# Performance work log

Measured on AMD Instinct MI355X. Metric: run time of the kernel, lower is better.

Reference implementation:

```python
import jax, jax.numpy as jnp
import numpy as np

GROUP = 128          # GPTQ quantization group size
H = 2048             # hidden_size
I = 1408             # moe_intermediate_size
T = 16384            # routed tokens


def _pack_rows(v):
    # v: [in, out] int4 values -> [in//8, out] int32 (8 nibbles per int32 along input dim)
    v = v.reshape(v.shape[0] // 8, 8, v.shape[1]).astype(jnp.int32)
    sh = (4 * jnp.arange(8, dtype=jnp.int32))[None, :, None]
    return (v << sh).sum(axis=1).astype(jnp.int32)


def _pack_cols(v):
    # v: [groups, out] int4 values -> [groups, out//8] int32
    v = v.reshape(v.shape[0], v.shape[1] // 8, 8).astype(jnp.int32)
    sh = (4 * jnp.arange(8, dtype=jnp.int32))[None, None, :]
    return (v << sh).sum(axis=-1).astype(jnp.int32)


def _unpack_rows(qw):
    # [in//8, out] int32 -> [in, out] int4 values
    sh = 4 * jnp.arange(8, dtype=jnp.int32)
    v = (qw[:, None, :] >> sh[None, :, None]) & 0xF
    return v.reshape(qw.shape[0] * 8, qw.shape[1])


def _unpack_cols(qz):
    # [groups, out//8] int32 -> [groups, out] int4 values
    sh = 4 * jnp.arange(8, dtype=jnp.int32)
    v = (qz[:, :, None] >> sh[None, None, :]) & 0xF
    return v.reshape(qz.shape[0], qz.shape[1] * 8)


def _dequant(qw, qz, sc):
    # GPTQ dequant: W[k, n] = (q[k, n] - (zero[g(k), n] + 1)) * scale[g(k), n]
    w = _unpack_rows(qw).astype(sc.dtype)                      # [in, out]
    z = (_unpack_cols(qz) + 1).astype(sc.dtype)                # [groups, out]
    scale = jnp.repeat(sc, GROUP, axis=0)                      # [in, out]
    zero = jnp.repeat(z, GROUP, axis=0)                        # [in, out]
    return (w - zero) * scale


def setup_inputs() -> dict:
    key = jax.random.key(0)
    ks = jax.random.split(key, 10)
    x = jax.random.normal(ks[0], (T, H), dtype=jnp.float32)

    def make_quant(kq, kz, ksc, n_in, n_out):
        q = jax.random.randint(kq, (n_in, n_out), 0, 16, dtype=jnp.int32)
        z = jax.random.randint(kz, (n_in // GROUP, n_out), 0, 15, dtype=jnp.int32)
        sc = jax.random.uniform(ksc, (n_in // GROUP, n_out), dtype=jnp.float32,
                                minval=1e-3, maxval=2e-2)
        return _pack_rows(q), _pack_cols(z), sc

    qw_g, qz_g, sc_g = make_quant(ks[1], ks[2], ks[3], H, I)
    qw_u, qz_u, sc_u = make_quant(ks[4], ks[5], ks[6], H, I)
    qw_d, qz_d, sc_d = make_quant(ks[7], ks[8], ks[9], I, H)
    return {"x": x,
            "qw_gate": qw_g, "qz_gate": qz_g, "sc_gate": sc_g,
            "qw_up": qw_u, "qz_up": qz_u, "sc_up": sc_u,
            "qw_down": qw_d, "qz_down": qz_d, "sc_down": sc_d}


def reference(x, qw_gate, qz_gate, sc_gate, qw_up, qz_up, sc_up,
              qw_down, qz_down, sc_down):
    Wg = _dequant(qw_gate, qz_gate, sc_gate)   # [H, I]
    Wu = _dequant(qw_up, qz_up, sc_up)         # [H, I]
    Wd = _dequant(qw_down, qz_down, sc_down)   # [I, H]
    # fused_gate_up: silu(x @ Wg) * (x @ Wu)
    h = jax.nn.silu(x @ Wg) * (x @ Wu)         # [T, I]
    return h @ Wd                              # [T, H]
```

## Files before the change

### kernel.cpp

```cpp
#include <hip/hip_runtime.h>

#define T_DIM 16384
#define H_DIM 2048
#define I_DIM 1408
#define NB_DIM (2 * I_DIM)

typedef _Float16 half8 __attribute__((ext_vector_type(8)));
typedef float floatx4 __attribute__((ext_vector_type(4)));

__device__ __forceinline__ void async_cp16(const _Float16* gp, _Float16* lp) {
    __builtin_amdgcn_global_load_lds(
        (const __attribute__((address_space(1))) unsigned int*)gp,
        (__attribute__((address_space(3))) unsigned int*)lp,
        16, 0, 0);
}

__global__ void cvt_fp16_kernel(const float* __restrict__ x, _Float16* __restrict__ xh) {
    int i = (blockIdx.x * 256 + threadIdx.x) * 8;
    const float4* p = (const float4*)(x + i);
    float4 a = p[0];
    float4 b = p[1];
    half8 o = { (_Float16)a.x, (_Float16)a.y, (_Float16)a.z, (_Float16)a.w,
                (_Float16)b.x, (_Float16)b.y, (_Float16)b.z, (_Float16)b.w };
    *(half8*)(xh + i) = o;
}

__global__ void dequant_kernel(const int* __restrict__ qw, const int* __restrict__ qz,
                               const float* __restrict__ sc, _Float16* __restrict__ Wt,
                               int K, int N, int interleave, int off) {
    __shared__ half8 tile[256];
    int t = threadIdx.x;
    int nl = t & 63, kl = t >> 6;
    int n  = blockIdx.x * 64 + nl;
    int kp = blockIdx.y * 4 + kl;
    int q = qw[kp * N + n];
    int g = kp >> 4;
    float scale = sc[g * N + n];
    int zq = (qz[g * (N >> 3) + (n >> 3)] >> (4 * (n & 7))) & 0xF;
    float zf = (float)(zq + 1);
    half8 o;
#pragma unroll
    for (int j = 0; j < 8; ++j)
        o[j] = (_Float16)(((float)((q >> (4 * j)) & 0xF) - zf) * scale);
    tile[nl * 4 + kl] = o;
    __syncthreads();
    int nl2 = t >> 2, kl2 = t & 3;
    int n2 = blockIdx.x * 64 + nl2;
    int np = interleave ? (((n2 >> 5) << 6) + (n2 & 31) + off) : n2;
    *(half8*)(Wt + (size_t)np * K + (size_t)(blockIdx.y * 4 + kl2) * 8) = tile[nl2 * 4 + kl2];
}


#define STAGE_A(p, h, kt) do {                                                        \
    async_cp16(ag + (size_t)((h) * 128) * KDIM + (size_t)(kt) * 64,                   \
               &As[p][(h) * 8192 + ldst]);                                            \
    async_cp16(ag + (size_t)((h) * 128 + 64) * KDIM + (size_t)(kt) * 64,              \
               &As[p][(h) * 8192 + 4096 + ldst]);                                     \
} while (0)

#define STAGE_B(p, h, kt) do {                                                        \
    async_cp16(bg + (size_t)((h) * 128) * KDIM + (size_t)(kt) * 64,                   \
               &Bs[p][(h) * 8192 + ldst]);                                            \
    async_cp16(bg + (size_t)((h) * 128 + 64) * KDIM + (size_t)(kt) * 64,              \
               &Bs[p][(h) * 8192 + 4096 + ldst]);                                     \
} while (0)

#define PHASE(p, mh, nh, RA, RB, STAGE_STMT, WAIT_STMT) do {                          \
    if (RA) {                                                                         \
        _Pragma("unroll") for (int i_ = 0; i_ < 4; ++i_)                              \
        _Pragma("unroll") for (int kk_ = 0; kk_ < 2; ++kk_)                           \
            af[i_][kk_] = *(const half8*)&As[p][(mh) * 4096 + (aoff[i_] ^ (kk_ * 32))]; \
    }                                                                                 \
    if (RB) {                                                                         \
        _Pragma("unroll") for (int j_ = 0; j_ < 2; ++j_)                              \
        _Pragma("unroll") for (int kk_ = 0; kk_ < 2; ++kk_)                           \
            bf[nh][j_][kk_] = *(const half8*)&Bs[p][(nh) * 2048 + (boff[j_] ^ (kk_ * 32))]; \
    }                                                                                 \
    STAGE_STMT;                                                                       \
    __builtin_amdgcn_s_barrier();                                                     \
    asm volatile("s_waitcnt lgkmcnt(0)" ::: "memory");                                \
    __builtin_amdgcn_s_setprio(1);                                                    \
    _Pragma("unroll") for (int kk_ = 0; kk_ < 2; ++kk_)                               \
    _Pragma("unroll") for (int i_ = 0; i_ < 4; ++i_)                                  \
    _Pragma("unroll") for (int j_ = 0; j_ < 2; ++j_)                                  \
        acc[(mh) * 4 + i_][(nh) * 2 + j_] = __builtin_amdgcn_mfma_f32_16x16x32_f16(   \
            af[i_][kk_], bf[nh][j_][kk_], acc[(mh) * 4 + i_][(nh) * 2 + j_], 0, 0, 0);\
    __builtin_amdgcn_s_setprio(0);                                                    \
    WAIT_STMT;                                                                        \
    __builtin_amdgcn_s_barrier();                                                     \
} while (0)

#define VM(n) asm volatile("s_waitcnt vmcnt(" #n ")" ::: "memory")

#define TILE_FULL(p, kt) do {                                                         \
    PHASE(p, 0, 0, 1, 1, STAGE_A(p ^ 1, 1, (kt) + 1), VM(6));                         \
    PHASE(p, 0, 1, 0, 1, STAGE_B(p ^ 1, 1, (kt) + 1), );                              \
    PHASE(p, 1, 0, 1, 0, STAGE_B(p, 0, (kt) + 2), );                                  \
    PHASE(p, 1, 1, 0, 0, STAGE_A(p, 0, (kt) + 2), VM(8));                             \
} while (0)

#define TILE_PEN(kt) do {                                                             \
    PHASE(0, 0, 0, 1, 1, STAGE_A(1, 1, (kt) + 1), VM(6));                             \
    PHASE(0, 0, 1, 0, 1, STAGE_B(1, 1, (kt) + 1), );                                  \
    PHASE(0, 1, 0, 1, 0, , );                                                         \
    PHASE(0, 1, 1, 0, 0, , VM(4));                                                    \
} while (0)

#define TILE_LAST() do {                                                              \
    PHASE(1, 0, 0, 1, 1, , VM(0));                                                    \
    PHASE(1, 0, 1, 0, 1, , );                                                         \
    PHASE(1, 1, 0, 1, 0, , );                                                         \
    PHASE(1, 1, 1, 0, 0, , );                                                         \
} while (0)

template<int KDIM, int EPI>
__launch_bounds__(512, 2)
__global__ void gemm256(const _Float16* __restrict__ A,
                        const _Float16* __restrict__ B,
                        void* __restrict__ Cout) {
    constexpr int NT = KDIM / 64;
    __shared__ __align__(16) _Float16 As[2][16384];
    __shared__ __align__(16) _Float16 Bs[2][16384];

    const int t = threadIdx.x;
    const int wave = t >> 6, lane = t & 63;
    const int id = blockIdx.x;
    const int m0 = (id & 63) * 256;
    const int n_p = id >> 6;
    const int n0 = n_p * 256;
    const int wm = wave >> 2, wn = wave & 3;
    const int q4 = lane >> 4, l15 = lane & 15;

    const int srow = wave * 8 + (lane >> 3);
    const int schunk = (lane & 7) ^ (lane >> 3);
    const _Float16* ag = A + (size_t)(m0 + srow) * KDIM + schunk * 8;
    const _Float16* bg = B + (size_t)(n0 + srow) * KDIM + schunk * 8;
    const int ldst = wave * 512;

    int aoff[4], boff[2];
#pragma unroll
    for (int i = 0; i < 4; ++i) {
        int rA = wm * 128 + i * 16 + l15;
        aoff[i] = rA * 64 + ((q4 ^ (rA & 7)) * 8);
    }
#pragma unroll
    for (int j = 0; j < 2; ++j) {
        int rB = wn * 64 + j * 16 + l15;
        boff[j] = rB * 64 + ((q4 ^ (rB & 7)) * 8);
    }

    floatx4 zero = {0.f, 0.f, 0.f, 0.f};
    floatx4 acc[8][4];
#pragma unroll
    for (int mi = 0; mi < 8; ++mi)
#pragma unroll
        for (int ni = 0; ni < 4; ++ni) acc[mi][ni] = zero;

    half8 af[4][2];
    half8 bf[2][2][2];

    STAGE_B(0, 0, 0);
    STAGE_A(0, 0, 0);
    STAGE_A(0, 1, 0);
    STAGE_B(0, 1, 0);
    STAGE_B(1, 0, 1);
    STAGE_A(1, 0, 1);
    VM(8);
    __builtin_amdgcn_s_barrier();

    for (int tt = 0; tt < NT - 2; tt += 2) {
        TILE_FULL(0, tt);
        TILE_FULL(1, tt + 1);
    }
    TILE_PEN(NT - 2);
    TILE_LAST();

    if constexpr (EPI == 1) {
        _Float16* hout = (_Float16*)Cout;
        const int rbase = m0 + wm * 128 + q4 * 4;
        const int colbase = (n_p * 4 + wn) * 32 + l15;
#pragma unroll
        for (int mi = 0; mi < 8; ++mi)
#pragma unroll
            for (int nc = 0; nc < 2; ++nc)
#pragma unroll
                for (int r = 0; r < 4; ++r) {
                    int row = rbase + mi * 16 + r;
                    int col = colbase + nc * 16;
                    float g = acc[mi][nc][r];
                    float u = acc[mi][nc + 2][r];
                    float s = (g / (1.0f + __expf(-g))) * u;
                    hout[(size_t)row * I_DIM + col] = (_Float16)s;
                }
    } else {
        float* outp = (float*)Cout;
        const int rbase = m0 + wm * 128 + q4 * 4;
#pragma unroll
        for (int mi = 0; mi < 8; ++mi)
#pragma unroll
            for (int ni = 0; ni < 4; ++ni)
#pragma unroll
                for (int r = 0; r < 4; ++r) {
                    int row = rbase + mi * 16 + r;
                    int col = n0 + wn * 64 + ni * 16 + l15;
                    outp[(size_t)row * H_DIM + col] = acc[mi][ni][r];
                }
    }
}

extern "C" void kernel_launch(void* const* d_in, const int* in_sizes, int n_in,
                              void* d_out, int out_size, void* d_ws, size_t ws_size,
                              hipStream_t stream) {
    const float* x    = (const float*)d_in[0];
    const int* qw_g   = (const int*)d_in[1];
    const int* qz_g   = (const int*)d_in[2];
    const float* sc_g = (const float*)d_in[3];
    const int* qw_u   = (const int*)d_in[4];
    const int* qz_u   = (const int*)d_in[5];
    const float* sc_u = (const float*)d_in[6];
    const int* qw_d   = (const int*)d_in[7];
    const int* qz_d   = (const int*)d_in[8];
    const float* sc_d = (const float*)d_in[9];
    float* out = (float*)d_out;

    char* ws = (char*)d_ws;
    _Float16* xh  = (_Float16*)ws;  ws += (size_t)T_DIM * H_DIM * sizeof(_Float16);
    _Float16* hh  = (_Float16*)ws;  ws += (size_t)T_DIM * I_DIM * sizeof(_Float16);
    _Float16* Bgu = (_Float16*)ws;  ws += (size_t)NB_DIM * H_DIM * sizeof(_Float16);
    _Float16* Wd  = (_Float16*)ws;  ws += (size_t)I_DIM * H_DIM * sizeof(_Float16);

    cvt_fp16_kernel<<<(T_DIM * H_DIM) / 2048, 256, 0, stream>>>(x, xh);
    dequant_kernel<<<dim3(I_DIM / 64, H_DIM / 32), 256, 0, stream>>>(qw_g, qz_g, sc_g, Bgu, H_DIM, I_DIM, 1, 0);
    dequant_kernel<<<dim3(I_DIM / 64, H_DIM / 32), 256, 0, stream>>>(qw_u, qz_u, sc_u, Bgu, H_DIM, I_DIM, 1, 32);
    dequant_kernel<<<dim3(H_DIM / 64, I_DIM / 32), 256, 0, stream>>>(qw_d, qz_d, sc_d, Wd, I_DIM, H_DIM, 0, 0);
    gemm256<H_DIM, 1><<<(T_DIM / 256) * (NB_DIM / 256), 512, 0, stream>>>(xh, Bgu, hh);
    gemm256<I_DIM, 0><<<(T_DIM / 256) * (H_DIM / 256), 512, 0, stream>>>(hh, Wd, out);
}
```

Measured before the change: 497.8 us.

## Restructure GEMM main loop with inline-asm LDS reads and reordered prefetch schedule

```diff
diff --git a/kernel.cpp b/kernel.cpp
--- a/kernel.cpp
+++ b/kernel.cpp
@@ -51,66 +51,69 @@
 }
 
 
-#define STAGE_A(p, h, kt) do {                                                        \
-    async_cp16(ag + (size_t)((h) * 128) * KDIM + (size_t)(kt) * 64,                   \
-               &As[p][(h) * 8192 + ldst]);                                            \
-    async_cp16(ag + (size_t)((h) * 128 + 64) * KDIM + (size_t)(kt) * 64,              \
-               &As[p][(h) * 8192 + 4096 + ldst]);                                     \
-} while (0)
-
-#define STAGE_B(p, h, kt) do {                                                        \
+#define STAGE_A2(pp, sub, kt) do {                                                    \
+    async_cp16(ag + (size_t)((sub) * 64) * KDIM + (size_t)(kt) * 64,                  \
+               &As[pp][(sub) * 4096 + ldst]);                                         \
+    async_cp16(ag + (size_t)(128 + (sub) * 64) * KDIM + (size_t)(kt) * 64,            \
+               &As[pp][8192 + (sub) * 4096 + ldst]);                                  \
+} while (0)
+
+#define STAGE_B(pp, h, kt) do {                                                       \
     async_cp16(bg + (size_t)((h) * 128) * KDIM + (size_t)(kt) * 64,                   \
-               &Bs[p][(h) * 8192 + ldst]);                                            \
+               &Bs[pp][(h) * 8192 + ldst]);                                           \
     async_cp16(bg + (size_t)((h) * 128 + 64) * KDIM + (size_t)(kt) * 64,              \
-               &Bs[p][(h) * 8192 + 4096 + ldst]);                                     \
-} while (0)
-
-#define PHASE(p, mh, nh, RA, RB, STAGE_STMT, WAIT_STMT) do {                          \
-    if (RA) {                                                                         \
-        _Pragma("unroll") for (int i_ = 0; i_ < 4; ++i_)                              \
-        _Pragma("unroll") for (int kk_ = 0; kk_ < 2; ++kk_)                           \
-            af[i_][kk_] = *(const half8*)&As[p][(mh) * 4096 + (aoff[i_] ^ (kk_ * 32))]; \
+               &Bs[pp][(h) * 8192 + 4096 + ldst]);                                    \
+} while (0)
+
+#define DSR(dst, a, OFF) \
+    asm volatile("ds_read_b128 %0, %1 offset:%2" : "=v"(dst) : "v"(a), "n"(OFF) : "memory")
+
+#define READ_A(pp, mh) do {                                                           \
+    _Pragma("unroll") for (int i_ = 0; i_ < 4; ++i_) {                                \
+        DSR(af[i_][0], aw[i_][0], (pp) * 32768 + (mh) * 8192);                        \
+        DSR(af[i_][1], aw[i_][1], (pp) * 32768 + (mh) * 8192);                        \
     }                                                                                 \
-    if (RB) {                                                                         \
-        _Pragma("unroll") for (int j_ = 0; j_ < 2; ++j_)                              \
-        _Pragma("unroll") for (int kk_ = 0; kk_ < 2; ++kk_)                           \
-            bf[nh][j_][kk_] = *(const half8*)&Bs[p][(nh) * 2048 + (boff[j_] ^ (kk_ * 32))]; \
+} while (0)
+
+#define READ_B(pp, nh) do {                                                           \
+    _Pragma("unroll") for (int j_ = 0; j_ < 2; ++j_) {                                \
+        DSR(bf[nh][j_][0], bw[j_][0], (pp) * 32768 + (nh) * 4096);                    \
+        DSR(bf[nh][j_][1], bw[j_][1], (pp) * 32768 + (nh) * 4096);                    \
     }                                                                                 \
-    STAGE_STMT;                                                                       \
-    __builtin_amdgcn_s_barrier();                                                     \
-    asm volatile("s_waitcnt lgkmcnt(0)" ::: "memory");                                \
-    __builtin_amdgcn_s_setprio(1);                                                    \
+} while (0)
+
+#define MFMA16(mh, nh)                                                                \
     _Pragma("unroll") for (int kk_ = 0; kk_ < 2; ++kk_)                               \
     _Pragma("unroll") for (int i_ = 0; i_ < 4; ++i_)                                  \
     _Pragma("unroll") for (int j_ = 0; j_ < 2; ++j_)                                  \
         acc[(mh) * 4 + i_][(nh) * 2 + j_] = __builtin_amdgcn_mfma_f32_16x16x32_f16(   \
-            af[i_][kk_], bf[nh][j_][kk_], acc[(mh) * 4 + i_][(nh) * 2 + j_], 0, 0, 0);\
-    __builtin_amdgcn_s_setprio(0);                                                    \
-    WAIT_STMT;                                                                        \
-    __builtin_amdgcn_s_barrier();                                                     \
-} while (0)
-
+            af[i_][kk_], bf[nh][j_][kk_], acc[(mh) * 4 + i_][(nh) * 2 + j_], 0, 0, 0)
+
+#define LG(n) asm volatile("s_waitcnt lgkmcnt(" #n ")" ::: "memory")
 #define VM(n) asm volatile("s_waitcnt vmcnt(" #n ")" ::: "memory")
+#define BAR __builtin_amdgcn_s_barrier()
+#define SB0 __builtin_amdgcn_sched_barrier(0)
+#define PRIO1 __builtin_amdgcn_s_setprio(1)
+#define PRIO0 __builtin_amdgcn_s_setprio(0)
 
 #define TILE_FULL(p, kt) do {                                                         \
-    PHASE(p, 0, 0, 1, 1, STAGE_A(p ^ 1, 1, (kt) + 1), VM(6));                         \
-    PHASE(p, 0, 1, 0, 1, STAGE_B(p ^ 1, 1, (kt) + 1), );                              \
-    PHASE(p, 1, 0, 1, 0, STAGE_B(p, 0, (kt) + 2), );                                  \
-    PHASE(p, 1, 1, 0, 0, STAGE_A(p, 0, (kt) + 2), VM(8));                             \
-} while (0)
-
-#define TILE_PEN(kt) do {                                                             \
-    PHASE(0, 0, 0, 1, 1, STAGE_A(1, 1, (kt) + 1), VM(6));                             \
-    PHASE(0, 0, 1, 0, 1, STAGE_B(1, 1, (kt) + 1), );                                  \
-    PHASE(0, 1, 0, 1, 0, , );                                                         \
-    PHASE(0, 1, 1, 0, 0, , VM(4));                                                    \
+     STAGE_A2(p ^ 1, 0, (kt) + 1);                                           \
+    BAR; LG(4); SB0; PRIO1; MFMA16(0, 0); PRIO0; SB0;                                 \
+     STAGE_B(p ^ 1, 0, (kt) + 1); STAGE_B(p ^ 1, 1, (kt) + 1);               \
+    VM(6); BAR; LG(0); SB0; PRIO1; MFMA16(0, 1); PRIO0; SB0;                          \
+    READ_A(p, 1);                                                                     \
+     STAGE_A2(p ^ 1, 1, (kt) + 1);                                           \
+    BAR; LG(0); SB0; PRIO1; MFMA16(1, 0); PRIO0; SB0;                                 \
+     VM(2); BAR; LG(0); SB0; PRIO1; MFMA16(1, 1); PRIO0; SB0;                \
+    READ_A(p ^ 1, 0); READ_B(p ^ 1, 0); READ_B(p ^ 1, 1);                             \
 } while (0)
 
 #define TILE_LAST() do {                                                              \
-    PHASE(1, 0, 0, 1, 1, , VM(0));                                                    \
-    PHASE(1, 0, 1, 0, 1, , );                                                         \
-    PHASE(1, 1, 0, 1, 0, , );                                                         \
-    PHASE(1, 1, 1, 0, 0, , );                                                         \
+    BAR; LG(4); SB0; PRIO1; MFMA16(0, 0); PRIO0; SB0;                                 \
+    VM(0); BAR; LG(0); SB0; PRIO1; MFMA16(0, 1); PRIO0; SB0;                          \
+    READ_A(1, 1);                                                                     \
+    BAR; LG(0); SB0; PRIO1; MFMA16(1, 0); PRIO0; SB0;                                 \
+    BAR; LG(0); SB0; PRIO1; MFMA16(1, 1); PRIO0; SB0;                                 \
 } while (0)
 
 template<int KDIM, int EPI>
@@ -137,16 +140,22 @@
     const _Float16* bg = B + (size_t)(n0 + srow) * KDIM + schunk * 8;
     const int ldst = wave * 512;
 
-    int aoff[4], boff[2];
+    unsigned AsB = (unsigned)(uintptr_t)&As[0][0];
+    unsigned BsB = (unsigned)(uintptr_t)&Bs[0][0];
+    unsigned aw[4][2], bw[2][2];
 #pragma unroll
     for (int i = 0; i < 4; ++i) {
         int rA = wm * 128 + i * 16 + l15;
-        aoff[i] = rA * 64 + ((q4 ^ (rA & 7)) * 8);
+        unsigned e = (unsigned)(rA * 64 + ((q4 ^ (rA & 7)) * 8)) * 2u;
+        aw[i][0] = AsB + e;
+        aw[i][1] = AsB + (e ^ 64u);
     }
 #pragma unroll
     for (int j = 0; j < 2; ++j) {
         int rB = wn * 64 + j * 16 + l15;
-        boff[j] = rB * 64 + ((q4 ^ (rB & 7)) * 8);
+        unsigned e = (unsigned)(rB * 64 + ((q4 ^ (rB & 7)) * 8)) * 2u;
+        bw[j][0] = BsB + e;
+        bw[j][1] = BsB + (e ^ 64u);
     }
 
     floatx4 zero = {0.f, 0.f, 0.f, 0.f};
@@ -159,20 +168,19 @@
     half8 af[4][2];
     half8 bf[2][2][2];
 
+    STAGE_A2(0, 0, 0);
     STAGE_B(0, 0, 0);
-    STAGE_A(0, 0, 0);
-    STAGE_A(0, 1, 0);
     STAGE_B(0, 1, 0);
-    STAGE_B(1, 0, 1);
-    STAGE_A(1, 0, 1);
-    VM(8);
-    __builtin_amdgcn_s_barrier();
+    STAGE_A2(0, 1, 0);
+    VM(2);
+    BAR;
+    READ_A(0, 0); READ_B(0, 0); READ_B(0, 1);
 
     for (int tt = 0; tt < NT - 2; tt += 2) {
         TILE_FULL(0, tt);
         TILE_FULL(1, tt + 1);
     }
-    TILE_PEN(NT - 2);
+    TILE_FULL(0, NT - 2);
     TILE_LAST();
 
     if constexpr (EPI == 1) {
```

Result: no change. 498.1 us (+0.1%).
